# Optimization experiments

Measured on AMD Instinct MI355X. Metric: run time of the kernel, lower is better.

Reference implementation:

```python
import jax, jax.numpy as jnp
from jax import lax
import numpy as np

H, W = 64, 64
K = 5                 # LO_kernel_size
SIGMA = 0.5           # LO_sigma
CHAN_PER_POS = 8
INIT_STRIDE = 16
BATCH = 32


def _num_offsets(h, w, s):
    ny = (h - s) // s * 2 + 1
    nx = (w - s) // s * 2 + 1
    return ny, nx, ny * nx - 1  # use_origin=False drops (0,0)


def setup_inputs() -> dict:
    key = jax.random.key(0)
    k1, k2 = jax.random.split(key)
    ny, nx, npos = _num_offsets(H, W, INIT_STRIDE)
    C = npos * CHAN_PER_POS
    x = jax.random.normal(k1, (BATCH, C, H, W), dtype=jnp.float32)
    # init_offset(): grid of (iw*stride, ih*stride), skipping origin
    offs = []
    for ih in range(-(ny // 2), ny // 2 + 1):
        for iw in range(-(nx // 2), nx // 2 + 1):
            if ih == 0 and iw == 0:
                continue
            offs.append([iw * INIT_STRIDE, ih * INIT_STRIDE])
    offset = jnp.asarray(np.array(offs, dtype=np.float32))
    # perturb so suboffsets (fractional part) are nonzero, as after training
    offset = offset + jax.random.uniform(k2, offset.shape, dtype=jnp.float32,
                                         minval=-0.4, maxval=0.4)
    return {"x": x, "offset": offset}


def _displace(x, off_int):
    # x: (B, P, Cpp, H, W); off_int: (P, 2) int32 (dx, dy)
    # out[y, x] = in[y - dy, x - dx], zero outside (integer shift by +offset)
    _, _, _, h, w = x.shape

    def shift_one(xp, dxy):
        dx, dy = dxy[0], dxy[1]
        ys = jnp.arange(h) - dy
        xs = jnp.arange(w) - dx
        ym = (ys >= 0) & (ys < h)
        xm = (xs >= 0) & (xs < w)
        ysc = jnp.clip(ys, 0, h - 1)
        xsc = jnp.clip(xs, 0, w - 1)
        out = xp[:, :, ysc][:, :, :, xsc]
        return out * (ym[:, None] & xm[None, :]).astype(xp.dtype)

    return jax.vmap(shift_one, in_axes=(1, 0), out_axes=1)(x, off_int)


def reference(x, offset) -> jnp.ndarray:
    B, C, h, w = x.shape
    P = offset.shape[0]
    cpp = C // P  # bind_chan

    off_round = jnp.round(offset)
    off_int = off_round.astype(jnp.int32)

    # integer-part displacement per channel group
    disp = _displace(x.reshape(B, P, cpp, h, w), off_int).reshape(B, C, h, w)

    # fractional part -> gaussian interpolation kernel (offset.dim()==2 path)
    sub = offset - lax.stop_gradient(off_round)          # (P, 2) = (subx, suby)
    c = K // 2
    jj, ii = jnp.meshgrid(jnp.arange(K, dtype=jnp.float32) - c,
                          jnp.arange(K, dtype=jnp.float32) - c, indexing='xy')
    field = jnp.stack([jj, ii], axis=-1)                 # (K, K, 2): (x, y)
    d = field[None] + sub[:, None, None, :]              # (P, K, K, 2)
    kernel = jnp.exp(-jnp.sum(d * d, axis=-1) / (2.0 * SIGMA ** 2))
    kernel = kernel / jnp.sum(kernel, axis=(1, 2), keepdims=True)

    # depthwise conv: each per-position kernel shared by bind_chan channels
    kw = jnp.repeat(kernel, cpp, axis=0)[:, None]        # (C, 1, K, K)
    out = lax.conv_general_dilated(
        disp, kw, window_strides=(1, 1), padding=[(c, c), (c, c)],
        feature_group_count=C,
        dimension_numbers=('NCHW', 'OIHW', 'NCHW'))
    return out
```

## Files before the change

### kernel.cpp

```cpp
#include <hip/hip_runtime.h>
#include <math.h>

#define HH 64
#define WW 64
#define KS 5
#define CPP 8
#define NPOS 48
#define CHAN (NPOS * CPP)
#define NBATCH 32

__device__ __forceinline__ float dpp_shr1(float v) {
    return __int_as_float(__builtin_amdgcn_mov_dpp(__float_as_int(v), 0x138, 0xF, 0xF, true));
}
__device__ __forceinline__ float dpp_shl1(float v) {
    return __int_as_float(__builtin_amdgcn_mov_dpp(__float_as_int(v), 0x130, 0xF, 0xF, true));
}

__global__ __launch_bounds__(256)
void displace_dpp_kernel(const float* __restrict__ x,
                         const float* __restrict__ off,
                         float* __restrict__ out)
{
    const int t    = threadIdx.x;
    const int lane = t & 63;
    const int plane = __builtin_amdgcn_readfirstlane(blockIdx.x * 4 + (t >> 6));
    const int p = (plane % CHAN) / CPP;

    const float* __restrict__ src = x   + (size_t)plane * (HH * WW);
    float*       __restrict__ dst = out + (size_t)plane * (HH * WW);

    const float offx = off[2 * p + 0];
    const float offy = off[2 * p + 1];
    const float rxf = rintf(offx), ryf = rintf(offy);
    const int   dx = (int)rxf,     dy = (int)ryf;
    const float subx = offx - rxf, suby = offy - ryf;

    float wxr[KS], wy[KS];
    float sumx = 0.f, sumy = 0.f;
    #pragma unroll
    for (int k = 0; k < KS; ++k) {
        const float ax = (float)(k - 2) + subx;
        const float ay = (float)(k - 2) + suby;
        wxr[k] = __expf(-2.0f * ax * ax);
        wy[k]  = __expf(-2.0f * ay * ay);
        sumx += wxr[k];
        sumy += wy[k];
    }
    const float inv = 1.0f / (sumx * sumy);

    float wxm[KS];
    #pragma unroll
    for (int k = 0; k < KS; ++k) {
        const int sl = lane + (k - 2);
        wxm[k] = ((unsigned)sl < (unsigned)WW) ? wxr[k] * inv : 0.0f;
    }

    const int   sx  = lane - dx;
    const float mx  = ((unsigned)sx < (unsigned)WW) ? 1.0f : 0.0f;
    const int   sxc = min(max(sx, 0), WW - 1);

    float hb[5];

    #pragma unroll
    for (int i = 0; i < HH + 4; ++i) {
        const int  yy = i - 2;
        const int  sy = yy - dy;
        const bool rowok = (((unsigned)yy < (unsigned)HH) & ((unsigned)sy < (unsigned)HH));
        const int  syc = min(max(sy, 0), HH - 1);

        const float v   = src[syc * WW + sxc] * mx;
        const float sm1 = dpp_shr1(v);
        const float sm2 = dpp_shr1(sm1);
        const float sp1 = dpp_shl1(v);
        const float sp2 = dpp_shl1(sp1);

        float h = wxm[0] * sm2;
        h = fmaf(wxm[1], sm1, h);
        h = fmaf(wxm[2], v,   h);
        h = fmaf(wxm[3], sp1, h);
        h = fmaf(wxm[4], sp2, h);
        hb[i % 5] = rowok ? h : 0.0f;

        if (i >= 4) {
            const int y = i - 4;
            float a = wy[0] * hb[(i - 4) % 5];
            a = fmaf(wy[1], hb[(i - 3) % 5], a);
            a = fmaf(wy[2], hb[(i - 2) % 5], a);
            a = fmaf(wy[3], hb[(i - 1) % 5], a);
            a = fmaf(wy[4], hb[(i - 0) % 5], a);
            dst[y * WW + lane] = a;
        }
    }
}

extern "C" void kernel_launch(void* const* d_in, const int* in_sizes, int n_in,
                              void* d_out, int out_size, void* d_ws, size_t ws_size,
                              hipStream_t stream) {
    const float* x   = (const float*)d_in[0];
    const float* off = (const float*)d_in[1];
    float* out = (float*)d_out;

    const int blocks = NBATCH * CHAN / 4;
    displace_dpp_kernel<<<blocks, 256, 0, stream>>>(x, off, out);
}
```

Measured before the change: 318.8 us.

## Stage rows through LDS with float4 loads and stores, prefetching next row group

Each wave now loads four input rows at a time with 16-byte vector loads into per-wave LDS and prefetches the next group while computing on the current one. Lanes read their shifted pixels from LDS, and output rows are staged in LDS and written back as float4 stores. This replaces one scalar 4-byte global load and store per lane per row. The aim is fewer, wider memory transactions and more loads in flight. The launch bound also gains a minimum-occupancy hint, at the cost of added LDS traffic and per-wave shared memory.

```diff
diff --git a/kernel.cpp b/kernel.cpp
--- a/kernel.cpp
+++ b/kernel.cpp
@@ -16,15 +16,21 @@
     return __int_as_float(__builtin_amdgcn_mov_dpp(__float_as_int(v), 0x130, 0xF, 0xF, true));
 }
 
-__global__ __launch_bounds__(256)
+__global__ __launch_bounds__(256, 4)
 void displace_dpp_kernel(const float* __restrict__ x,
                          const float* __restrict__ off,
                          float* __restrict__ out)
 {
     const int t    = threadIdx.x;
     const int lane = t & 63;
-    const int plane = __builtin_amdgcn_readfirstlane(blockIdx.x * 4 + (t >> 6));
+    const int wid  = t >> 6;
+    const int plane = __builtin_amdgcn_readfirstlane(blockIdx.x * 4 + wid);
     const int p = (plane % CHAN) / CPP;
+
+    __shared__ __align__(16) float lin [4][4][WW];
+    __shared__ __align__(16) float lout[4][4][WW];
+    float (* __restrict__ inbuf)[WW]  = lin[wid];
+    float (* __restrict__ outbuf)[WW] = lout[wid];
 
     const float* __restrict__ src = x   + (size_t)plane * (HH * WW);
     float*       __restrict__ dst = out + (size_t)plane * (HH * WW);
@@ -59,36 +65,65 @@
     const float mx  = ((unsigned)sx < (unsigned)WW) ? 1.0f : 0.0f;
     const int   sxc = min(max(sx, 0), WW - 1);
 
+    const int g  = lane >> 4;
+    const int pq = lane & 15;
+
     float hb[5];
 
+    float4 cur;
+    {
+        const int yy  = -2 + g;
+        const int sy  = yy - dy;
+        const int syc = min(max(sy, 0), HH - 1);
+        cur = *reinterpret_cast<const float4*>(src + syc * WW + pq * 4);
+    }
+
     #pragma unroll
-    for (int i = 0; i < HH + 4; ++i) {
-        const int  yy = i - 2;
-        const int  sy = yy - dy;
-        const bool rowok = (((unsigned)yy < (unsigned)HH) & ((unsigned)sy < (unsigned)HH));
-        const int  syc = min(max(sy, 0), HH - 1);
+    for (int j = 0; j < 17; ++j) {
+        *reinterpret_cast<float4*>(&inbuf[g][pq * 4]) = cur;
 
-        const float v   = src[syc * WW + sxc] * mx;
-        const float sm1 = dpp_shr1(v);
-        const float sm2 = dpp_shr1(sm1);
-        const float sp1 = dpp_shl1(v);
-        const float sp2 = dpp_shl1(sp1);
+        if (j < 16) {
+            const int yy  = 4 * (j + 1) - 2 + g;
+            const int sy  = yy - dy;
+            const int syc = min(max(sy, 0), HH - 1);
+            cur = *reinterpret_cast<const float4*>(src + syc * WW + pq * 4);
+        }
 
-        float h = wxm[0] * sm2;
-        h = fmaf(wxm[1], sm1, h);
-        h = fmaf(wxm[2], v,   h);
-        h = fmaf(wxm[3], sp1, h);
-        h = fmaf(wxm[4], sp2, h);
-        hb[i % 5] = rowok ? h : 0.0f;
+        #pragma unroll
+        for (int r = 0; r < 4; ++r) {
+            const int  i  = 4 * j + r;
+            const int  yy = i - 2;
+            const int  sy = yy - dy;
+            const bool rowok = (((unsigned)yy < (unsigned)HH) &
+                                ((unsigned)sy < (unsigned)HH));
 
-        if (i >= 4) {
-            const int y = i - 4;
-            float a = wy[0] * hb[(i - 4) % 5];
-            a = fmaf(wy[1], hb[(i - 3) % 5], a);
-            a = fmaf(wy[2], hb[(i - 2) % 5], a);
-            a = fmaf(wy[3], hb[(i - 1) % 5], a);
-            a = fmaf(wy[4], hb[(i - 0) % 5], a);
-            dst[y * WW + lane] = a;
+            const float v   = inbuf[r][sxc] * mx;
+            const float sm1 = dpp_shr1(v);
+            const float sm2 = dpp_shr1(sm1);
+            const float sp1 = dpp_shl1(v);
+            const float sp2 = dpp_shl1(sp1);
+
+            float h = wxm[0] * sm2;
+            h = fmaf(wxm[1], sm1, h);
+            h = fmaf(wxm[2], v,   h);
+            h = fmaf(wxm[3], sp1, h);
+            h = fmaf(wxm[4], sp2, h);
+            hb[i % 5] = rowok ? h : 0.0f;
+
+            if (i >= 4) {
+                float a = wy[0] * hb[(i - 4) % 5];
+                a = fmaf(wy[1], hb[(i - 3) % 5], a);
+                a = fmaf(wy[2], hb[(i - 2) % 5], a);
+                a = fmaf(wy[3], hb[(i - 1) % 5], a);
+                a = fmaf(wy[4], hb[(i - 0) % 5], a);
+                outbuf[r][lane] = a;
+            }
+        }
+
+        if (j >= 1) {
+            const int ybase = 4 * (j - 1);
+            const float4 o = *reinterpret_cast<const float4*>(&outbuf[g][pq * 4]);
+            *reinterpret_cast<float4*>(dst + (ybase + g) * WW + pq * 4) = o;
         }
     }
 }
```

After: 325.7 us. 1.02x slower.
